# Kernel tuning notes

Measured on AMD Instinct MI355X. Metric: run time of the kernel, lower is better.

Reference implementation:

```python
import jax, jax.numpy as jnp
import numpy as np

BATCH, N, DIM_IN, DIM_K, DIM_V, NH = 2, 4096, 256, 256, 256, 8

def setup_inputs() -> dict:
    key = jax.random.key(0)
    k1, k2, k3, k4 = jax.random.split(key, 4)
    s = 1.0 / np.sqrt(DIM_IN)
    return {
        "x": jax.random.normal(k1, (BATCH, N, DIM_IN), dtype=jnp.float32),
        "Wq": jax.random.normal(k2, (DIM_IN, DIM_K), dtype=jnp.float32) * s,
        "Wk": jax.random.normal(k3, (DIM_IN, DIM_K), dtype=jnp.float32) * s,
        "Wv": jax.random.normal(k4, (DIM_IN, DIM_V), dtype=jnp.float32) * s,
    }

def reference(x, Wq, Wk, Wv):
    b, n, _ = x.shape
    nh = NH
    dk = DIM_K // nh
    dv = DIM_V // nh
    # project and split heads: [b, nh, n, dk]
    q = jnp.einsum('bni,ik->bnk', x, Wq).reshape(b, n, nh, dk).transpose(0, 2, 1, 3)
    k = jnp.einsum('bni,ik->bnk', x, Wk).reshape(b, n, nh, dk).transpose(0, 2, 1, 3)
    v = jnp.einsum('bni,iv->bnv', x, Wv).reshape(b, n, nh, dv).transpose(0, 2, 1, 3)
    scale = 1.0 / np.sqrt(dk)
    dist = jnp.einsum('bhqd,bhkd->bhqk', q, k) * scale  # [b, nh, n, n]
    dist = jax.nn.softmax(dist, axis=-1)
    # dropout is identity in eval mode
    att = jnp.einsum('bhqk,bhkv->bhqv', dist, v)  # [b, nh, n, dv]
    return att.transpose(0, 2, 1, 3).reshape(b, n, DIM_V)
```

## Files before the change

kernel.cpp:

```cpp
#include <hip/hip_runtime.h>
#include <math.h>

#define BATCH 2
#define SEQ   4096
#define DIN   256
#define NH    8
#define DH    32
#define BH    (BATCH*NH)
#define NSPLIT 4
#define KRANGE (SEQ/NSPLIT)
#define TILES  (KRANGE/64)

typedef short bf16x8 __attribute__((ext_vector_type(8)));
typedef float f32x4  __attribute__((ext_vector_type(4)));

#if defined(__has_builtin)
#if __has_builtin(__builtin_amdgcn_exp2f)
#define EXP2(x) __builtin_amdgcn_exp2f(x)
#else
#define EXP2(x) exp2f(x)
#endif
#else
#define EXP2(x) exp2f(x)
#endif

#if defined(__has_builtin)
#if __has_builtin(__builtin_amdgcn_global_load_lds)
#define HAS_ASYNC_LDS 1
#endif
#endif

#define SC2 0.25508218f

__device__ __forceinline__ unsigned short f2bf(float f) {
    unsigned int u = __builtin_bit_cast(unsigned int, f);
    u += 0x7fffu + ((u >> 16) & 1u);
    return (unsigned short)(u >> 16);
}

__device__ __forceinline__ unsigned int pack_bf2(float f0, float f1) {
    unsigned int u0 = __builtin_bit_cast(unsigned int, f0) + 0x8000u;
    unsigned int u1 = __builtin_bit_cast(unsigned int, f1) + 0x8000u;
    return __builtin_amdgcn_perm(u1, u0, 0x07060302u);
}

__device__ __forceinline__ unsigned int pack_bf2_t(float f0, float f1) {
    return __builtin_amdgcn_perm(__builtin_bit_cast(unsigned int, f1),
                                 __builtin_bit_cast(unsigned int, f0),
                                 0x07060302u);
}

__device__ __forceinline__ void stage16(const unsigned short* g,
                                        unsigned short* lds_base, int lane) {
#ifdef HAS_ASYNC_LDS
    __builtin_amdgcn_global_load_lds(
        (const __attribute__((address_space(1))) unsigned int*)g,
        (__attribute__((address_space(3))) unsigned int*)lds_base, 16, 0, 0);
#else
    *(bf16x8*)(lds_base + (size_t)lane * 8) = *(const bf16x8*)g;
#endif
}

__global__ __launch_bounds__(256) void prep_kernel(
    const float* __restrict__ x,
    const float* __restrict__ Wq, const float* __restrict__ Wk, const float* __restrict__ Wv,
    unsigned short* __restrict__ xb, unsigned short* __restrict__ Wt)
{
    const int t = threadIdx.x;
    if (blockIdx.x < 2048) {
        int i4 = blockIdx.x * 256 + t;
        float4 v = ((const float4*)x)[i4];
        ushort4 o;
        o.x = f2bf(v.x); o.y = f2bf(v.y); o.z = f2bf(v.z); o.w = f2bf(v.w);
        ((ushort4*)xb)[i4] = o;
    } else {
        __shared__ float ws[64][65];
        int id   = blockIdx.x - 2048;
        int wsel = id >> 4;
        int tile = id & 15;
        int tr = (tile >> 2) * 64;
        int tc = (tile & 3) * 64;
        const float* __restrict__ W = (wsel == 0) ? Wq : (wsel == 1) ? Wk : Wv;
        #pragma unroll
        for (int i = 0; i < 16; i++) {
            int row = i * 4 + (t >> 6), col = t & 63;
            ws[row][col] = W[(size_t)(tr + row) * DIN + tc + col];
        }
        __syncthreads();
        unsigned short* dst = Wt + (size_t)wsel * DIN * DIN;
        #pragma unroll
        for (int i = 0; i < 16; i++) {
            int orow = i * 4 + (t >> 6), ocol = t & 63;
            dst[(size_t)(tc + orow) * DIN + tr + ocol] = f2bf(ws[ocol][orow]);
        }
    }
}

__global__ __launch_bounds__(256) void proj_kernel(
    const unsigned short* __restrict__ xb, const unsigned short* __restrict__ Wt,
    unsigned short* __restrict__ qh, unsigned short* __restrict__ kh,
    unsigned short* __restrict__ vt)
{
    __shared__ __align__(16) unsigned short abuf[8][4][64][8];
    __shared__ __align__(16) unsigned short bbuf[8][4][64][8];

    const int wsel = blockIdx.y;
    const int w    = threadIdx.x >> 6;
    const int lane = threadIdx.x & 63;
    const int quad = lane >> 4;
    const int l16  = lane & 15;

    const int sl   = lane ^ (lane >> 3);
    const int sl16 = sl >> 2, squad = sl & 3;
    const int s_ = (l16 << 2) | quad;
    const int jj = (s_ & 56) | ((s_ ^ (s_ >> 3)) & 7);

    int arow0, brow0;
    const unsigned short *Abase, *Bbase;
    if (wsel < 2) {
        int tt = blockIdx.x >> 7, nt = blockIdx.x & 127;
        arow0 = tt * 64; brow0 = nt * 64;
        Abase = Wt + (size_t)wsel * DIN * DIN + (size_t)arow0 * DIN;
        Bbase = xb + (size_t)brow0 * DIN;
    } else {
        int nt = blockIdx.x >> 2, tt = blockIdx.x & 3;
        arow0 = nt * 64; brow0 = tt * 64;
        Abase = xb + (size_t)arow0 * DIN;
        Bbase = Wt + (size_t)2 * DIN * DIN + (size_t)brow0 * DIN;
    }

    #pragma unroll
    for (int i = 0; i < 16; i++) {
        int id  = w * 16 + i;
        int isB = id >> 5, kb = (id >> 2) & 7, rt = id & 3;
        const unsigned short* src = (isB ? Bbase : Abase)
                                  + (size_t)(rt * 16 + sl16) * DIN + kb * 32 + squad * 8;
        unsigned short* dst = isB ? &bbuf[kb][rt][0][0] : &abuf[kb][rt][0][0];
        stage16(src, dst, lane);
    }
    __syncthreads();

    f32x4 acc[4];
    #pragma unroll
    for (int c = 0; c < 4; c++) acc[c] = (f32x4){0.f, 0.f, 0.f, 0.f};

    #pragma unroll
    for (int kb = 0; kb < 8; kb++) {
        bf16x8 af = *(const bf16x8*)&abuf[kb][w][jj][0];
        #pragma unroll
        for (int c = 0; c < 4; c++) {
            bf16x8 bfr = *(const bf16x8*)&bbuf[kb][c][jj][0];
            acc[c] = __builtin_amdgcn_mfma_f32_16x16x32_bf16(af, bfr, acc[c], 0, 0, 0);
        }
    }

    if (wsel < 2) {
        const float scl = (wsel == 0) ? SC2 : 1.0f;
        unsigned short* __restrict__ dst0 = (wsel == 0) ? qh : kh;
        const int t0 = arow0 + w * 16;
        const int h = t0 >> 5, d0 = (t0 & 31) + quad * 4;
        #pragma unroll
        for (int c = 0; c < 4; c++) {
            int n = brow0 + c * 16 + l16;
            int b = n >> 12, n12 = n & 4095;
            unsigned int u01 = pack_bf2(acc[c][0] * scl, acc[c][1] * scl);
            unsigned int u23 = pack_bf2(acc[c][2] * scl, acc[c][3] * scl);
            *(uint2*)&dst0[((size_t)(b * NH + h) * SEQ + n12) * DH + d0] = make_uint2(u01, u23);
        }
    } else {
        const int n0w = arow0 + w * 16;
        const int b = n0w >> 12, nbase = (n0w & 4095) + quad * 4;
        #pragma unroll
        for (int c = 0; c < 4; c++) {
            int t = brow0 + c * 16;
            int h = t >> 5, d = (t & 31) + l16;
            unsigned int u01 = pack_bf2(acc[c][0], acc[c][1]);
            unsigned int u23 = pack_bf2(acc[c][2], acc[c][3]);
            *(uint2*)&vt[((size_t)(b * NH + h) * DH + d) * SEQ + nbase] = make_uint2(u01, u23);
        }
    }
}

__global__ __launch_bounds__(256) void attn_kernel(
    const unsigned short* __restrict__ qh,
    const unsigned short* __restrict__ kh,
    const unsigned short* __restrict__ vt,
    float* __restrict__ po, float* __restrict__ pl)
{
    __shared__ __align__(16) unsigned short pbuf[4][16][64];
    __shared__ __align__(16) unsigned short kbuf[2][4][64][8];

    const int tid  = threadIdx.x;
    const int wave = tid >> 6;
    const int lane = tid & 63;
    const int quad = lane >> 4;
    const int l16  = lane & 15;
    const int sw   = l16 & 7;

    const int bh = blockIdx.x & 15;
    const int qb = (blockIdx.x >> 4) & 31;
    const int ks = blockIdx.x >> 9;
    const int q0 = qb * 128 + wave * 32;
    const int kbase = ks * KRANGE;

    const unsigned short* __restrict__ Qp = qh + (size_t)bh * SEQ * DH;
    const unsigned short* __restrict__ Kp = kh + (size_t)bh * SEQ * DH;
    const unsigned short* __restrict__ Vp = vt + (size_t)bh * DH * SEQ;

    const int sl    = lane ^ (lane >> 3);
    const int sl16  = sl >> 2, squad = sl & 3;
    const unsigned short* ksrc = Kp + (size_t)(kbase + wave * 16 + sl16) * DH + squad * 8;

    const int s_ = (l16 << 2) | quad;
    const int jj = (s_ & 56) | ((s_ ^ (s_ >> 3)) & 7);

    const unsigned short* vp0 = Vp + (size_t)l16 * SEQ + kbase + quad * 8;
    const unsigned short* vp1 = vp0 + (size_t)16 * SEQ;

    bf16x8 qf[2];
    qf[0] = *(const bf16x8*)(Qp + (size_t)(q0 +      l16) * DH + quad * 8);
    qf[1] = *(const bf16x8*)(Qp + (size_t)(q0 + 16 + l16) * DH + quad * 8);

    f32x4 o[2][2];
    #pragma unroll
    for (int i = 0; i < 2; i++)
        #pragma unroll
        for (int j = 0; j < 2; j++) o[i][j] = (f32x4){0.f, 0.f, 0.f, 0.f};
    f32x4 lacc[2] = {{0.f,0.f,0.f,0.f},{0.f,0.f,0.f,0.f}};
    const f32x4 z = {0.f, 0.f, 0.f, 0.f};

    stage16(ksrc, &kbuf[0][wave][0][0], lane);
    ksrc += 64 * DH;

    for (int t = 0; t < TILES; t++) {
        const int buf = t & 1;

        __syncthreads();

        if (t + 1 < TILES) {
            stage16(ksrc, &kbuf[buf ^ 1][wave][0][0], lane);
            ksrc += 64 * DH;
        }

        bf16x8 kf0 = *(const bf16x8*)&kbuf[buf][0][jj][0];
        bf16x8 kf1 = *(const bf16x8*)&kbuf[buf][1][jj][0];
        bf16x8 kf2 = *(const bf16x8*)&kbuf[buf][2][jj][0];
        bf16x8 kf3 = *(const bf16x8*)&kbuf[buf][3][jj][0];

        bf16x8 vf0 = *(const bf16x8*)(vp0);
        bf16x8 vf1 = *(const bf16x8*)(vp0 + 32);
        bf16x8 vf2 = *(const bf16x8*)(vp1);
        bf16x8 vf3 = *(const bf16x8*)(vp1 + 32);

        #pragma unroll
        for (int qt = 0; qt < 2; qt++) {
            bf16x8 kfs[4] = {kf0, kf1, kf2, kf3};
            #pragma unroll
            for (int c = 0; c < 4; c++) {
                f32x4 s = __builtin_amdgcn_mfma_f32_16x16x32_bf16(kfs[c], qf[qt], z, 0, 0, 0);
                float e0 = EXP2(s[0]);
                float e1 = EXP2(s[1]);
                float e2 = EXP2(s[2]);
                float e3 = EXP2(s[3]);
                lacc[qt] += (f32x4){e0, e1, e2, e3};
                int chs = ((c * 2 + (quad >> 1)) ^ sw) * 8 + (quad & 1) * 4;
                *(uint2*)&pbuf[wave][l16][chs] =
                    make_uint2(pack_bf2_t(e0, e1), pack_bf2_t(e2, e3));
            }
            bf16x8 pf0 = *(const bf16x8*)&pbuf[wave][l16][((0 + quad) ^ sw) * 8];
            bf16x8 pf1 = *(const bf16x8*)&pbuf[wave][l16][((4 + quad) ^ sw) * 8];
            o[qt][0] = __builtin_amdgcn_mfma_f32_16x16x32_bf16(pf0, vf0, o[qt][0], 0, 0, 0);
            o[qt][0] = __builtin_amdgcn_mfma_f32_16x16x32_bf16(pf1, vf1, o[qt][0], 0, 0, 0);
            o[qt][1] = __builtin_amdgcn_mfma_f32_16x16x32_bf16(pf0, vf2, o[qt][1], 0, 0, 0);
            o[qt][1] = __builtin_amdgcn_mfma_f32_16x16x32_bf16(pf1, vf3, o[qt][1], 0, 0, 0);
        }

        vp0 += 64;
        vp1 += 64;
    }

    const size_t obase = (size_t)(ks * BH + bh) * SEQ;
    #pragma unroll
    for (int qt = 0; qt < 2; qt++) {
        float rs = (lacc[qt][0] + lacc[qt][1]) + (lacc[qt][2] + lacc[qt][3]);
        rs += __shfl_xor(rs, 16);
        rs += __shfl_xor(rs, 32);
        if (quad == 0) pl[obase + q0 + qt * 16 + l16] = rs;
        #pragma unroll
        for (int r = 0; r < 4; r++) {
            int n = q0 + qt * 16 + quad * 4 + r;
            float* dst = po + (obase + n) * DH;
            dst[l16]      = o[qt][0][r];
            dst[16 + l16] = o[qt][1][r];
        }
    }
}

__global__ __launch_bounds__(256) void merge_kernel(
    const float* __restrict__ po, const float* __restrict__ pl,
    float* __restrict__ out)
{
    int t    = blockIdx.x * 256 + threadIdx.x;
    int d8   = t & 7;
    int pair = t >> 3;
    int bh   = pair >> 12;
    int n    = pair & 4095;
    float4 s = {0.f, 0.f, 0.f, 0.f};
    float ls = 0.f;
    #pragma unroll
    for (int sp = 0; sp < NSPLIT; sp++) {
        size_t base = (size_t)(sp * BH + bh) * SEQ + n;
        float4 v = ((const float4*)(po + base * DH))[d8];
        s.x += v.x; s.y += v.y; s.z += v.z; s.w += v.w;
        ls += pl[base];
    }
    float inv = 1.f / ls;
    int b = bh >> 3, h = bh & 7;
    float4 o = {s.x * inv, s.y * inv, s.z * inv, s.w * inv};
    ((float4*)(out + ((size_t)b * SEQ + n) * (NH * DH) + h * DH))[d8] = o;
}

extern "C" void kernel_launch(void* const* d_in, const int* in_sizes, int n_in,
                              void* d_out, int out_size, void* d_ws, size_t ws_size,
                              hipStream_t stream)
{
    const float* x  = (const float*)d_in[0];
    const float* Wq = (const float*)d_in[1];
    const float* Wk = (const float*)d_in[2];
    const float* Wv = (const float*)d_in[3];
    float* out = (float*)d_out;

    unsigned short* qh = (unsigned short*)d_ws;
    unsigned short* kh = qh + (size_t)BH * SEQ * DH;
    unsigned short* vt = kh + (size_t)BH * SEQ * DH;
    unsigned short* xb = vt + (size_t)BH * SEQ * DH;
    unsigned short* Wt = xb + (size_t)BATCH * SEQ * DIN;
    float* po = (float*)(Wt + 3 * DIN * DIN);
    float* pl = po + (size_t)NSPLIT * BH * SEQ * DH;

    prep_kernel<<<dim3(2096), 256, 0, stream>>>(x, Wq, Wk, Wv, xb, Wt);
    proj_kernel<<<dim3(512, 3), 256, 0, stream>>>(xb, Wt, qh, kh, vt);
    attn_kernel<<<dim3(BH * (SEQ / 128) * NSPLIT), 256, 0, stream>>>(qh, kh, vt, po, pl);
    merge_kernel<<<dim3(2048), 256, 0, stream>>>(po, pl, out);
}
```

Before: 152.2 us.

## Stage V through LDS, compute row sums via MFMA, store bf16 partials

Attention kernel now stages V tiles into double-buffered LDS with async global-to-LDS loads, the same way as K, instead of reading them directly from global memory per lane. The softmax denominator is computed by extra MFMAs against a ones vector instead of VALU accumulation plus shuffles. Partial outputs are written as bf16, which halves merge traffic, and launch bounds request 4 blocks per CU. The risks are lower precision in the partial sums and the cost of the extra MFMAs and LDS space.

```diff
diff --git a/kernel.cpp b/kernel.cpp
--- a/kernel.cpp
+++ b/kernel.cpp
@@ -18,16 +18,18 @@
 #if __has_builtin(__builtin_amdgcn_exp2f)
 #define EXP2(x) __builtin_amdgcn_exp2f(x)
 #else
-#define EXP2(x) exp2f(x)
+#define EXP2_ASM 1
 #endif
 #else
-#define EXP2(x) exp2f(x)
-#endif
-
-#if defined(__has_builtin)
-#if __has_builtin(__builtin_amdgcn_global_load_lds)
-#define HAS_ASYNC_LDS 1
-#endif
+#define EXP2_ASM 1
+#endif
+#ifdef EXP2_ASM
+__device__ __forceinline__ float exp2_raw(float x) {
+    float r;
+    asm("v_exp_f32 %0, %1\n\ts_nop 1" : "=v"(r) : "v"(x));
+    return r;
+}
+#define EXP2(x) exp2_raw(x)
 #endif
 
 #define SC2 0.25508218f
@@ -49,6 +51,12 @@
                                  __builtin_bit_cast(unsigned int, f0),
                                  0x07060302u);
 }
+
+#if defined(__has_builtin)
+#if __has_builtin(__builtin_amdgcn_global_load_lds)
+#define HAS_ASYNC_LDS 1
+#endif
+#endif
 
 __device__ __forceinline__ void stage16(const unsigned short* g,
                                         unsigned short* lds_base, int lane) {
@@ -181,14 +189,15 @@
     }
 }
 
-__global__ __launch_bounds__(256) void attn_kernel(
+__global__ __launch_bounds__(256, 4) void attn_kernel(
     const unsigned short* __restrict__ qh,
     const unsigned short* __restrict__ kh,
     const unsigned short* __restrict__ vt,
-    float* __restrict__ po, float* __restrict__ pl)
+    unsigned short* __restrict__ po, float* __restrict__ pl)
 {
     __shared__ __align__(16) unsigned short pbuf[4][16][64];
     __shared__ __align__(16) unsigned short kbuf[2][4][64][8];
+    __shared__ __align__(16) unsigned short vbuf[2][4][64][8];
 
     const int tid  = threadIdx.x;
     const int wave = tid >> 6;
@@ -210,27 +219,32 @@
     const int sl    = lane ^ (lane >> 3);
     const int sl16  = sl >> 2, squad = sl & 3;
     const unsigned short* ksrc = Kp + (size_t)(kbase + wave * 16 + sl16) * DH + squad * 8;
+    const int vdh = wave >> 1, vkh = wave & 1;
+    const unsigned short* vsrc = Vp + (size_t)(vdh * 16 + sl16) * SEQ + kbase + vkh * 32 + squad * 8;
 
     const int s_ = (l16 << 2) | quad;
     const int jj = (s_ & 56) | ((s_ ^ (s_ >> 3)) & 7);
-
-    const unsigned short* vp0 = Vp + (size_t)l16 * SEQ + kbase + quad * 8;
-    const unsigned short* vp1 = vp0 + (size_t)16 * SEQ;
 
     bf16x8 qf[2];
     qf[0] = *(const bf16x8*)(Qp + (size_t)(q0 +      l16) * DH + quad * 8);
     qf[1] = *(const bf16x8*)(Qp + (size_t)(q0 + 16 + l16) * DH + quad * 8);
 
+    const bf16x8 ones = {0x3F80, 0x3F80, 0x3F80, 0x3F80, 0x3F80, 0x3F80, 0x3F80, 0x3F80};
+
     f32x4 o[2][2];
-    #pragma unroll
-    for (int i = 0; i < 2; i++)
-        #pragma unroll
-        for (int j = 0; j < 2; j++) o[i][j] = (f32x4){0.f, 0.f, 0.f, 0.f};
-    f32x4 lacc[2] = {{0.f,0.f,0.f,0.f},{0.f,0.f,0.f,0.f}};
+    f32x4 lones[2];
+    #pragma unroll
+    for (int i = 0; i < 2; i++) {
+        o[i][0] = (f32x4){0.f, 0.f, 0.f, 0.f};
+        o[i][1] = (f32x4){0.f, 0.f, 0.f, 0.f};
+        lones[i] = (f32x4){0.f, 0.f, 0.f, 0.f};
+    }
     const f32x4 z = {0.f, 0.f, 0.f, 0.f};
 
     stage16(ksrc, &kbuf[0][wave][0][0], lane);
+    stage16(vsrc, &vbuf[0][wave][0][0], lane);
     ksrc += 64 * DH;
+    vsrc += 64;
 
     for (int t = 0; t < TILES; t++) {
         const int buf = t & 1;
@@ -239,65 +253,61 @@
 
         if (t + 1 < TILES) {
             stage16(ksrc, &kbuf[buf ^ 1][wave][0][0], lane);
+            stage16(vsrc, &vbuf[buf ^ 1][wave][0][0], lane);
             ksrc += 64 * DH;
-        }
-
-        bf16x8 kf0 = *(const bf16x8*)&kbuf[buf][0][jj][0];
-        bf16x8 kf1 = *(const bf16x8*)&kbuf[buf][1][jj][0];
-        bf16x8 kf2 = *(const bf16x8*)&kbuf[buf][2][jj][0];
-        bf16x8 kf3 = *(const bf16x8*)&kbuf[buf][3][jj][0];
-
-        bf16x8 vf0 = *(const bf16x8*)(vp0);
-        bf16x8 vf1 = *(const bf16x8*)(vp0 + 32);
-        bf16x8 vf2 = *(const bf16x8*)(vp1);
-        bf16x8 vf3 = *(const bf16x8*)(vp1 + 32);
+            vsrc += 64;
+        }
+
+        bf16x8 kf[4], vf[4];
+        #pragma unroll
+        for (int c = 0; c < 4; c++) kf[c] = *(const bf16x8*)&kbuf[buf][c][jj][0];
+        #pragma unroll
+        for (int f = 0; f < 4; f++) vf[f] = *(const bf16x8*)&vbuf[buf][f][jj][0];
 
         #pragma unroll
         for (int qt = 0; qt < 2; qt++) {
-            bf16x8 kfs[4] = {kf0, kf1, kf2, kf3};
             #pragma unroll
             for (int c = 0; c < 4; c++) {
-                f32x4 s = __builtin_amdgcn_mfma_f32_16x16x32_bf16(kfs[c], qf[qt], z, 0, 0, 0);
+                f32x4 s = __builtin_amdgcn_mfma_f32_16x16x32_bf16(kf[c], qf[qt], z, 0, 0, 0);
                 float e0 = EXP2(s[0]);
                 float e1 = EXP2(s[1]);
                 float e2 = EXP2(s[2]);
                 float e3 = EXP2(s[3]);
-                lacc[qt] += (f32x4){e0, e1, e2, e3};
                 int chs = ((c * 2 + (quad >> 1)) ^ sw) * 8 + (quad & 1) * 4;
                 *(uint2*)&pbuf[wave][l16][chs] =
                     make_uint2(pack_bf2_t(e0, e1), pack_bf2_t(e2, e3));
             }
             bf16x8 pf0 = *(const bf16x8*)&pbuf[wave][l16][((0 + quad) ^ sw) * 8];
             bf16x8 pf1 = *(const bf16x8*)&pbuf[wave][l16][((4 + quad) ^ sw) * 8];
-            o[qt][0] = __builtin_amdgcn_mfma_f32_16x16x32_bf16(pf0, vf0, o[qt][0], 0, 0, 0);
-            o[qt][0] = __builtin_amdgcn_mfma_f32_16x16x32_bf16(pf1, vf1, o[qt][0], 0, 0, 0);
-            o[qt][1] = __builtin_amdgcn_mfma_f32_16x16x32_bf16(pf0, vf2, o[qt][1], 0, 0, 0);
-            o[qt][1] = __builtin_amdgcn_mfma_f32_16x16x32_bf16(pf1, vf3, o[qt][1], 0, 0, 0);
-        }
-
-        vp0 += 64;
-        vp1 += 64;
+            o[qt][0] = __builtin_amdgcn_mfma_f32_16x16x32_bf16(pf0, vf[0], o[qt][0], 0, 0, 0);
+            o[qt][0] = __builtin_amdgcn_mfma_f32_16x16x32_bf16(pf1, vf[1], o[qt][0], 0, 0, 0);
+            o[qt][1] = __builtin_amdgcn_mfma_f32_16x16x32_bf16(pf0, vf[2], o[qt][1], 0, 0, 0);
+            o[qt][1] = __builtin_amdgcn_mfma_f32_16x16x32_bf16(pf1, vf[3], o[qt][1], 0, 0, 0);
+            lones[qt] = __builtin_amdgcn_mfma_f32_16x16x32_bf16(pf0, ones, lones[qt], 0, 0, 0);
+            lones[qt] = __builtin_amdgcn_mfma_f32_16x16x32_bf16(pf1, ones, lones[qt], 0, 0, 0);
+        }
     }
 
     const size_t obase = (size_t)(ks * BH + bh) * SEQ;
     #pragma unroll
     for (int qt = 0; qt < 2; qt++) {
-        float rs = (lacc[qt][0] + lacc[qt][1]) + (lacc[qt][2] + lacc[qt][3]);
-        rs += __shfl_xor(rs, 16);
-        rs += __shfl_xor(rs, 32);
-        if (quad == 0) pl[obase + q0 + qt * 16 + l16] = rs;
+        if (l16 == 0) {
+            #pragma unroll
+            for (int r = 0; r < 4; r++)
+                pl[obase + q0 + qt * 16 + quad * 4 + r] = lones[qt][r];
+        }
         #pragma unroll
         for (int r = 0; r < 4; r++) {
             int n = q0 + qt * 16 + quad * 4 + r;
-            float* dst = po + (obase + n) * DH;
-            dst[l16]      = o[qt][0][r];
-            dst[16 + l16] = o[qt][1][r];
+            unsigned short* dst = po + (obase + n) * DH;
+            dst[l16]      = f2bf(o[qt][0][r]);
+            dst[16 + l16] = f2bf(o[qt][1][r]);
         }
     }
 }
 
 __global__ __launch_bounds__(256) void merge_kernel(
-    const float* __restrict__ po, const float* __restrict__ pl,
+    const unsigned short* __restrict__ po, const float* __restrict__ pl,
     float* __restrict__ out)
 {
     int t    = blockIdx.x * 256 + threadIdx.x;
@@ -305,18 +315,20 @@
     int pair = t >> 3;
     int bh   = pair >> 12;
     int n    = pair & 4095;
-    float4 s = {0.f, 0.f, 0.f, 0.f};
-    float ls = 0.f;
+    float s0 = 0.f, s1 = 0.f, s2 = 0.f, s3 = 0.f, ls = 0.f;
     #pragma unroll
     for (int sp = 0; sp < NSPLIT; sp++) {
         size_t base = (size_t)(sp * BH + bh) * SEQ + n;
-        float4 v = ((const float4*)(po + base * DH))[d8];
-        s.x += v.x; s.y += v.y; s.z += v.z; s.w += v.w;
+        uint2 v = ((const uint2*)(po + base * DH))[d8];
+        s0 += __builtin_bit_cast(float, v.x << 16);
+        s1 += __builtin_bit_cast(float, v.x & 0xFFFF0000u);
+        s2 += __builtin_bit_cast(float, v.y << 16);
+        s3 += __builtin_bit_cast(float, v.y & 0xFFFF0000u);
         ls += pl[base];
     }
     float inv = 1.f / ls;
     int b = bh >> 3, h = bh & 7;
-    float4 o = {s.x * inv, s.y * inv, s.z * inv, s.w * inv};
+    float4 o = {s0 * inv, s1 * inv, s2 * inv, s3 * inv};
     ((float4*)(out + ((size_t)b * SEQ + n) * (NH * DH) + h * DH))[d8] = o;
 }
 
@@ -335,8 +347,8 @@
     unsigned short* vt = kh + (size_t)BH * SEQ * DH;
     unsigned short* xb = vt + (size_t)BH * SEQ * DH;
     unsigned short* Wt = xb + (size_t)BATCH * SEQ * DIN;
-    float* po = (float*)(Wt + 3 * DIN * DIN);
-    float* pl = po + (size_t)NSPLIT * BH * SEQ * DH;
+    unsigned short* po = Wt + 3 * DIN * DIN;
+    float* pl = (float*)(po + (size_t)NSPLIT * BH * SEQ * DH);
 
     prep_kernel<<<dim3(2096), 256, 0, stream>>>(x, Wq, Wk, Wv, xb, Wt);
     proj_kernel<<<dim3(512, 3), 256, 0, stream>>>(xb, Wt, qh, kh, vt);
```

Result: faster. 137.6 us (-9.6%).
